# Kernel optimization log

Hardware: AMD Instinct MI355X
Metric: run time of the kernel (lower is better)

Reference implementation:

```python
import jax, jax.numpy as jnp
import numpy as np

TOP_K = 2  # num_experts_per_tok


def setup_inputs() -> dict:
    key = jax.random.key(0)
    ks = jax.random.split(key, 5)
    B, T, D, E, F = 2, 2048, 1024, 8, 2048
    scale_d = 1.0 / np.sqrt(D)
    scale_f = 1.0 / np.sqrt(F)
    return {
        "x": jax.random.normal(ks[0], (B, T, D), jnp.float32),
        "kernel_router_DE": jax.random.normal(ks[1], (D, E), jnp.float32) * scale_d,
        "kernel_gating_EDF": jax.random.normal(ks[2], (E, D, F), jnp.float32) * scale_d,
        "kernel_up_EDF": jax.random.normal(ks[3], (E, D, F), jnp.float32) * scale_d,
        "kernel_down_EFD": jax.random.normal(ks[4], (E, F, D), jnp.float32) * scale_f,
    }


def reference(x, kernel_router_DE, kernel_gating_EDF, kernel_up_EDF, kernel_down_EFD):
    E = kernel_router_DE.shape[-1]
    x = x.astype(jnp.float32)

    # --- Router: logits -> softmax -> top_k -> renormalize with softmax ---
    router_logits_BTE = jnp.einsum('BTD,DE->BTE', x, kernel_router_DE)
    probs_BTE = jax.nn.softmax(router_logits_BTE.astype(jnp.float32), axis=-1)
    weights_BTX, indices_BTX = jax.lax.top_k(probs_BTE, TOP_K)
    norm_weights_BTX = jax.nn.softmax(weights_BTX, axis=-1)

    # --- Scatter top-k weights back to dense per-expert weights ---
    one_hot_BTXE = jax.nn.one_hot(indices_BTX, num_classes=E, dtype=jnp.float32)
    full_weights_BTE = jnp.sum(one_hot_BTXE * norm_weights_BTX[..., None], axis=2)

    # --- Dense all-expert MLP (gating * up -> down), weighted combine ---
    gating_BTEF = jnp.einsum('BTD,EDF->BTEF', x, kernel_gating_EDF)
    fuse_BTEF = jax.nn.silu(gating_BTEF) * jnp.einsum('BTD,EDF->BTEF', x, kernel_up_EDF)
    down_BTED = jnp.einsum('BTEF,EFD->BTED', fuse_BTEF, kernel_down_EFD)
    out_BTD = jnp.einsum('BTED,BTE->BTD', down_BTED, full_weights_BTE)
    return out_BTD.astype(jnp.float32)
```

## Files before the change

### kernel.cpp

```cpp
#include <hip/hip_runtime.h>
#include <cstdint>

#define N_TOK 4096
#define DIM   1024
#define NEXP  8
#define FDIM  2048

typedef _Float16 f16_t;
typedef _Float16 f16x8 __attribute__((ext_vector_type(8)));
typedef float    f32x4 __attribute__((ext_vector_type(4)));

__device__ inline unsigned packh(float a, float b) {
    union { f16_t h[2]; unsigned u; } p;
    p.h[0] = (f16_t)a; p.h[1] = (f16_t)b;
    return p.u;
}

__device__ inline void gl2lds16(const void* g, void* l) {
    __builtin_amdgcn_global_load_lds(
        (const __attribute__((address_space(1))) unsigned*)g,
        (__attribute__((address_space(3))) unsigned*)l, 16, 0, 0);
}

__global__ __launch_bounds__(256) void prep_kernel(
    const float* __restrict__ x, const float* __restrict__ wr,
    float* __restrict__ topw, int* __restrict__ counts, int* __restrict__ bucket,
    f16_t* __restrict__ xf,
    const float* __restrict__ wg, const float* __restrict__ wu,
    f16_t* __restrict__ wgT, f16_t* __restrict__ wuT)
{
    __shared__ union { float r[NEXP][DIM]; unsigned sP[64][68]; } sm;
    __shared__ int sIdx[32];
    int tid = threadIdx.x;

    if (blockIdx.x >= 256) {
        int b2 = blockIdx.x - 256;
        int m = b2 >> 8;
        int tix = b2 & 255;
        const float* in; f16_t* out;
        if (m < 8) { in = wg + (size_t)m * DIM * FDIM;       out = wgT + (size_t)m * DIM * FDIM; }
        else       { in = wu + (size_t)(m - 8) * DIM * FDIM; out = wuT + (size_t)(m - 8) * DIM * FDIM; }
        int rb = (tix & 7) * 128;
        int cb = (tix >> 3) * 64;
        int dp = tid >> 2;
        int fc = (tid & 3) * 16;
        const float* r0 = in + (size_t)(rb + 2 * dp) * FDIM + cb + fc;
        const float* r1 = r0 + FDIM;
#pragma unroll
        for (int j = 0; j < 16; j += 4) {
            float4 a = *(const float4*)(r0 + j);
            float4 b = *(const float4*)(r1 + j);
            sm.sP[fc + j + 0][dp] = packh(a.x, b.x);
            sm.sP[fc + j + 1][dp] = packh(a.y, b.y);
            sm.sP[fc + j + 2][dp] = packh(a.z, b.z);
            sm.sP[fc + j + 3][dp] = packh(a.w, b.w);
        }
        __syncthreads();
        int c = tid >> 2;
        int rc = tid & 3;
        uint4* dst = (uint4*)(out + (size_t)(cb + c) * DIM + rb + rc * 32);
        const unsigned* src = &sm.sP[c][rc * 16];
#pragma unroll
        for (int j = 0; j < 4; j++)
            dst[j] = *(const uint4*)(src + j * 4);
        return;
    }

    int blk = blockIdx.x;
    {
        const float* xblk = x + (size_t)blk * 16 * DIM;
        f16_t* xfblk = xf + (size_t)blk * 16 * DIM;
#pragma unroll
        for (int i = tid; i < 16 * DIM / 8; i += 256) {
            float4 a = ((const float4*)xblk)[2 * i];
            float4 b = ((const float4*)xblk)[2 * i + 1];
            union { f16_t h[8]; uint4 u; } pk;
            pk.h[0] = (f16_t)a.x; pk.h[1] = (f16_t)a.y; pk.h[2] = (f16_t)a.z; pk.h[3] = (f16_t)a.w;
            pk.h[4] = (f16_t)b.x; pk.h[5] = (f16_t)b.y; pk.h[6] = (f16_t)b.z; pk.h[7] = (f16_t)b.w;
            ((uint4*)xfblk)[i] = pk.u;
        }
    }
    for (int i = tid; i < DIM * NEXP / 4; i += 256) {
        float4 v = ((const float4*)wr)[i];
        int base = i * 4;
        sm.r[(base + 0) & 7][(base + 0) >> 3] = v.x;
        sm.r[(base + 1) & 7][(base + 1) >> 3] = v.y;
        sm.r[(base + 2) & 7][(base + 2) >> 3] = v.z;
        sm.r[(base + 3) & 7][(base + 3) >> 3] = v.w;
    }
    __syncthreads();
    int wave = tid >> 6, lane = tid & 63;
    int t0 = blk * 16 + wave * 4;
    for (int tt = 0; tt < 4; ++tt) {
        int t = t0 + tt;
        float acc[NEXP];
#pragma unroll
        for (int e = 0; e < NEXP; e++) acc[e] = 0.f;
        const float* xr = x + (size_t)t * DIM;
#pragma unroll
        for (int k = 0; k < DIM / 64; k++) {
            int d = lane + k * 64;
            float xv = xr[d];
#pragma unroll
            for (int e = 0; e < NEXP; e++) acc[e] += xv * sm.r[e][d];
        }
#pragma unroll
        for (int e = 0; e < NEXP; e++) {
#pragma unroll
            for (int off = 32; off > 0; off >>= 1)
                acc[e] += __shfl_xor(acc[e], off, 64);
        }
        if (lane == 0) {
            float mx = acc[0];
#pragma unroll
            for (int e = 1; e < NEXP; e++) mx = fmaxf(mx, acc[e]);
            float p[NEXP]; float s = 0.f;
#pragma unroll
            for (int e = 0; e < NEXP; e++) { p[e] = expf(acc[e] - mx); s += p[e]; }
            float inv = 1.f / s;
#pragma unroll
            for (int e = 0; e < NEXP; e++) p[e] *= inv;
            int i1 = 0; float p1 = p[0];
#pragma unroll
            for (int e = 1; e < NEXP; e++) if (p[e] > p1) { p1 = p[e]; i1 = e; }
            int i2 = -1; float p2 = -1.f;
#pragma unroll
            for (int e = 0; e < NEXP; e++) if (e != i1 && p[e] > p2) { p2 = p[e]; i2 = e; }
            float e2 = expf(p2 - p1);
            float w1 = 1.f / (1.f + e2);
            topw[t * 2 + 0] = w1;
            topw[t * 2 + 1] = e2 * w1;
            int j = (wave * 4 + tt) * 2;
            sIdx[j + 0] = i1;
            sIdx[j + 1] = i2;
        }
    }
    __syncthreads();
    if (tid < NEXP) {
        int cnt = 0;
#pragma unroll
        for (int j = 0; j < 32; j++) cnt += (sIdx[j] == tid) ? 1 : 0;
        if (cnt > 0) {
            int pos = atomicAdd(&counts[tid * 32], cnt);
#pragma unroll
            for (int j = 0; j < 32; j++)
                if (sIdx[j] == tid)
                    bucket[tid * N_TOK + pos++] = (blk * 16 + (j >> 1)) * 2 + (j & 1);
        }
    }
}

__global__ __launch_bounds__(256) void gateup_kernel(
    const f16_t* __restrict__ xf,
    const f16_t* __restrict__ wgT, const f16_t* __restrict__ wuT,
    const int* __restrict__ counts, const int* __restrict__ bucket,
    f16_t* __restrict__ H)
{
    int flat = blockIdx.x;
    int e = flat & 7;
    int idx = flat >> 3;
    int m0 = (idx & 31) * 128;
    int n0 = (idx >> 5) * 64;
    int cnt = counts[e * 32];
    if (m0 >= cnt) return;

    __shared__ f16_t sA[128 * 32];
    __shared__ f16_t sBg[64 * 32];
    __shared__ f16_t sBu[64 * 32];
    __shared__ int sEnt[128];

    int tid = threadIdx.x;
    if (tid < 128) {
        int i = m0 + tid;
        sEnt[tid] = bucket[e * N_TOK + (i < cnt ? i : m0)];
    }
    __syncthreads();

    int wave = tid >> 6, lane = tid & 63;
    int q = ((lane & 3) - (lane >> 3)) & 3;
    int rA0 = wave * 32 + (lane >> 2);
    int rA1 = rA0 + 16;
    int rB  = wave * 16 + (lane >> 2);
    const f16_t* gA0 = xf + (size_t)(sEnt[rA0] >> 1) * DIM + q * 8;
    const f16_t* gA1 = xf + (size_t)(sEnt[rA1] >> 1) * DIM + q * 8;
    const f16_t* gBg = wgT + ((size_t)e * FDIM + n0 + rB) * DIM + q * 8;
    const f16_t* gBu = wuT + ((size_t)e * FDIM + n0 + rB) * DIM + q * 8;
    f16_t* lA0 = &sA[wave * 1024 + lane * 8];
    f16_t* lA1 = lA0 + 512;
    f16_t* lBg = &sBg[wave * 512 + lane * 8];
    f16_t* lBu = &sBu[wave * 512 + lane * 8];

    f32x4 accG[4][2], accU[4][2];
    f32x4 zero = {0.f, 0.f, 0.f, 0.f};
#pragma unroll
    for (int i = 0; i < 4; i++)
#pragma unroll
        for (int j = 0; j < 2; j++) { accG[i][j] = zero; accU[i][j] = zero; }

    int wm = (wave & 1) * 64, wn = (wave >> 1) * 32;
    int fm = lane & 15, quad = lane >> 4;
    int p8 = ((quad + (fm >> 1)) & 3) * 8;

    for (int k0 = 0; k0 < DIM; k0 += 32) {
        gl2lds16(gA0 + k0, lA0);
        gl2lds16(gA1 + k0, lA1);
        gl2lds16(gBg + k0, lBg);
        gl2lds16(gBu + k0, lBu);
        __syncthreads();
        f16x8 af[4], bg[2], bu[2];
#pragma unroll
        for (int mi = 0; mi < 4; mi++)
            af[mi] = *(const f16x8*)&sA[(wm + mi * 16 + fm) * 32 + p8];
#pragma unroll
        for (int ni = 0; ni < 2; ni++) {
            bg[ni] = *(const f16x8*)&sBg[(wn + ni * 16 + fm) * 32 + p8];
            bu[ni] = *(const f16x8*)&sBu[(wn + ni * 16 + fm) * 32 + p8];
        }
#pragma unroll
        for (int mi = 0; mi < 4; mi++)
#pragma unroll
            for (int ni = 0; ni < 2; ni++) {
                accG[mi][ni] = __builtin_amdgcn_mfma_f32_16x16x32_f16(af[mi], bg[ni], accG[mi][ni], 0, 0, 0);
                accU[mi][ni] = __builtin_amdgcn_mfma_f32_16x16x32_f16(af[mi], bu[ni], accU[mi][ni], 0, 0, 0);
            }
        __syncthreads();
    }
    int crow = quad * 4, ccol = fm;
#pragma unroll
    for (int mi = 0; mi < 4; mi++) {
#pragma unroll
        for (int i = 0; i < 4; i++) {
            int m = wm + mi * 16 + crow + i;
            if (m0 + m < cnt) {
                int ent = sEnt[m];
                f16_t* hr = H + (size_t)ent * FDIM + n0 + wn;
#pragma unroll
                for (int ni = 0; ni < 2; ni++) {
                    float g = accG[mi][ni][i], u = accU[mi][ni][i];
                    float h = (g / (1.f + __expf(-g))) * u;
                    hr[ni * 16 + ccol] = (f16_t)h;
                }
            }
        }
    }
}

__global__ __launch_bounds__(256) void down_kernel(
    const f16_t* __restrict__ H, const float* __restrict__ wd,
    const int* __restrict__ counts, const int* __restrict__ bucket,
    const float* __restrict__ topw, float* __restrict__ out)
{
    int flat = blockIdx.x;
    int e = flat & 7;
    int idx = flat >> 3;
    int m0 = (idx & 31) * 128;
    int n0 = (idx >> 5) * 128;
    int cnt = counts[e * 32];
    if (m0 >= cnt) return;

    __shared__ f16_t sA[128 * 32];
    __shared__ f16_t sB[128 * 32];
    __shared__ int sEnt[128];

    int tid = threadIdx.x;
    if (tid < 128) {
        int i = m0 + tid;
        sEnt[tid] = bucket[e * N_TOK + (i < cnt ? i : m0)];
    }
    __syncthreads();

    int wave = tid >> 6, lane = tid & 63;
    int q = ((lane & 3) - (lane >> 3)) & 3;
    int r0 = wave * 32 + (lane >> 2);
    int r1 = r0 + 16;
    const f16_t* gA0 = H + (size_t)sEnt[r0] * FDIM + q * 8;
    const f16_t* gA1 = H + (size_t)sEnt[r1] * FDIM + q * 8;
    f16_t* lA0 = &sA[wave * 1024 + lane * 8];
    f16_t* lA1 = lA0 + 512;

    int fp = tid & 7;
    int dq = tid >> 3;
    int fp2 = fp * 2;
    const float* wde = wd + (size_t)e * FDIM * DIM + n0 + dq * 4;
    int o2 = (fp & 3) * 2;
    int g0 = (fp >> 2);
    int g1 = 2 + (fp >> 2);
    int cA = ((g0 ^ (dq & 3)) * 8) + o2;
    int cB = ((g1 ^ (dq & 3)) * 8) + o2;
    int rowb = dq * 4;

    float4 pb0, pb1, pb2, pb3;
#define LOADB(K0) {                                                             \
        const float* rr = wde + (size_t)((K0) + fp2) * DIM;                     \
        pb0 = *(const float4*)rr;                                               \
        pb1 = *(const float4*)(rr + DIM);                                       \
        pb2 = *(const float4*)(rr + 16 * DIM);                                  \
        pb3 = *(const float4*)(rr + 17 * DIM); }

    f32x4 acc[4][4];
    f32x4 zero = {0.f, 0.f, 0.f, 0.f};
#pragma unroll
    for (int i = 0; i < 4; i++)
#pragma unroll
        for (int j = 0; j < 4; j++) acc[i][j] = zero;

    int wm = (wave & 1) * 64, wn = (wave >> 1) * 64;
    int fm = lane & 15, quad = lane >> 4;
    int p8 = ((quad + (fm >> 1)) & 3) * 8;

    LOADB(0);
    for (int k0 = 0; k0 < FDIM; k0 += 32) {
        gl2lds16(gA0 + k0, lA0);
        gl2lds16(gA1 + k0, lA1);
        *(unsigned*)&sB[(rowb + 0) * 32 + cA] = packh(pb0.x, pb1.x);
        *(unsigned*)&sB[(rowb + 1) * 32 + cA] = packh(pb0.y, pb1.y);
        *(unsigned*)&sB[(rowb + 2) * 32 + cA] = packh(pb0.z, pb1.z);
        *(unsigned*)&sB[(rowb + 3) * 32 + cA] = packh(pb0.w, pb1.w);
        *(unsigned*)&sB[(rowb + 0) * 32 + cB] = packh(pb2.x, pb3.x);
        *(unsigned*)&sB[(rowb + 1) * 32 + cB] = packh(pb2.y, pb3.y);
        *(unsigned*)&sB[(rowb + 2) * 32 + cB] = packh(pb2.z, pb3.z);
        *(unsigned*)&sB[(rowb + 3) * 32 + cB] = packh(pb2.w, pb3.w);
        __syncthreads();
        if (k0 + 32 < FDIM) LOADB(k0 + 32);
        f16x8 af[4], bf[4];
#pragma unroll
        for (int mi = 0; mi < 4; mi++)
            af[mi] = *(const f16x8*)&sA[(wm + mi * 16 + fm) * 32 + p8];
#pragma unroll
        for (int ni = 0; ni < 4; ni++) {
            int row = wn + ni * 16 + fm;
            bf[ni] = *(const f16x8*)&sB[row * 32 + (quad ^ ((row >> 2) & 3)) * 8];
        }
#pragma unroll
        for (int mi = 0; mi < 4; mi++)
#pragma unroll
            for (int ni = 0; ni < 4; ni++)
                acc[mi][ni] = __builtin_amdgcn_mfma_f32_16x16x32_f16(af[mi], bf[ni], acc[mi][ni], 0, 0, 0);
        __syncthreads();
    }
#undef LOADB

    int crow = quad * 4, ccol = fm;
#pragma unroll
    for (int mi = 0; mi < 4; mi++) {
#pragma unroll
        for (int i = 0; i < 4; i++) {
            int m = wm + mi * 16 + crow + i;
            if (m0 + m < cnt) {
                int ent = sEnt[m];
                float w = topw[ent];
                float* orow = out + (size_t)(ent >> 1) * DIM + n0 + wn;
#pragma unroll
                for (int ni = 0; ni < 4; ni++)
                    atomicAdd(&orow[ni * 16 + ccol], w * acc[mi][ni][i]);
            }
        }
    }
}

extern "C" void kernel_launch(void* const* d_in, const int* in_sizes, int n_in,
                              void* d_out, int out_size, void* d_ws, size_t ws_size,
                              hipStream_t stream) {
    const float* x  = (const float*)d_in[0];
    const float* wr = (const float*)d_in[1];
    const float* wg = (const float*)d_in[2];
    const float* wu = (const float*)d_in[3];
    const float* wd = (const float*)d_in[4];
    float* out = (float*)d_out;
    char* ws = (char*)d_ws;
    const size_t MB = 1ull << 20;

    int*   counts = (int*)ws;
    int*   bucket = (int*)(ws + 1024);
    float* topw   = (float*)(ws + 160 * 1024);
    f16_t* xf     = (f16_t*)(ws + 1 * MB);
    f16_t* wgT    = (f16_t*)(ws + 9 * MB);
    f16_t* wuT    = (f16_t*)(ws + 41 * MB);
    f16_t* H      = (f16_t*)(ws + 73 * MB);

    hipMemsetAsync(counts, 0, 1024, stream);
    hipMemsetAsync(out, 0, out_size, stream);
    prep_kernel<<<4352, 256, 0, stream>>>(x, wr, topw, counts, bucket, xf, wg, wu, wgT, wuT);
    gateup_kernel<<<8192, 256, 0, stream>>>(xf, wgT, wuT, counts, bucket, H);
    down_kernel<<<2048, 256, 0, stream>>>(H, wd, counts, bucket, topw, out);
}
```

Baseline: 444.7 us.

## Pre-convert down-projection weights to transposed fp16 before the down GEMM

The down-projection weights are now converted once per call into a transposed fp16 copy. This happens either inside the prep kernel, when the workspace is large enough, or in a separate conversion kernel that reuses the xf region. The down kernel then streams the B operand with direct global-to-LDS loads, in place of register-staged fp32 loads that were repacked in every k-iteration. This cuts the per-tile fp32 traffic and repack work, since the conversion is not repeated across the many M-tiles. In exchange it adds a full weight conversion pass and extra workspace traffic.

```diff
diff --git a/kernel.cpp b/kernel.cpp
--- a/kernel.cpp
+++ b/kernel.cpp
@@ -27,7 +27,8 @@
     float* __restrict__ topw, int* __restrict__ counts, int* __restrict__ bucket,
     f16_t* __restrict__ xf,
     const float* __restrict__ wg, const float* __restrict__ wu,
-    f16_t* __restrict__ wgT, f16_t* __restrict__ wuT)
+    const float* __restrict__ wd,
+    f16_t* __restrict__ wgT, f16_t* __restrict__ wuT, f16_t* __restrict__ wdT)
 {
     __shared__ union { float r[NEXP][DIM]; unsigned sP[64][68]; } sm;
     __shared__ int sIdx[32];
@@ -38,14 +39,22 @@
         int m = b2 >> 8;
         int tix = b2 & 255;
         const float* in; f16_t* out;
-        if (m < 8) { in = wg + (size_t)m * DIM * FDIM;       out = wgT + (size_t)m * DIM * FDIM; }
-        else       { in = wu + (size_t)(m - 8) * DIM * FDIM; out = wuT + (size_t)(m - 8) * DIM * FDIM; }
-        int rb = (tix & 7) * 128;
-        int cb = (tix >> 3) * 64;
+        int R, C, tiles_r;
+        if (m < 16) {
+            R = DIM; C = FDIM; tiles_r = DIM / 128;
+            if (m < 8) { in = wg + (size_t)m * DIM * FDIM;       out = wgT + (size_t)m * DIM * FDIM; }
+            else       { in = wu + (size_t)(m - 8) * DIM * FDIM; out = wuT + (size_t)(m - 8) * DIM * FDIM; }
+        } else {
+            R = FDIM; C = DIM; tiles_r = FDIM / 128;
+            in = wd + (size_t)(m - 16) * FDIM * DIM;
+            out = wdT + (size_t)(m - 16) * FDIM * DIM;
+        }
+        int rb = (tix % tiles_r) * 128;
+        int cb = (tix / tiles_r) * 64;
         int dp = tid >> 2;
         int fc = (tid & 3) * 16;
-        const float* r0 = in + (size_t)(rb + 2 * dp) * FDIM + cb + fc;
-        const float* r1 = r0 + FDIM;
+        const float* r0 = in + (size_t)(rb + 2 * dp) * C + cb + fc;
+        const float* r1 = r0 + C;
 #pragma unroll
         for (int j = 0; j < 16; j += 4) {
             float4 a = *(const float4*)(r0 + j);
@@ -58,7 +67,7 @@
         __syncthreads();
         int c = tid >> 2;
         int rc = tid & 3;
-        uint4* dst = (uint4*)(out + (size_t)(cb + c) * DIM + rb + rc * 32);
+        uint4* dst = (uint4*)(out + (size_t)(cb + c) * R + rb + rc * 32);
         const unsigned* src = &sm.sP[c][rc * 16];
 #pragma unroll
         for (int j = 0; j < 4; j++)
@@ -148,6 +157,41 @@
                     bucket[tid * N_TOK + pos++] = (blk * 16 + (j >> 1)) * 2 + (j & 1);
         }
     }
+}
+
+__global__ __launch_bounds__(256) void wdcvt_kernel(
+    const float* __restrict__ wd, f16_t* __restrict__ wdT)
+{
+    __shared__ unsigned sP[64][68];
+    int m = blockIdx.y;
+    const float* in = wd + (size_t)m * FDIM * DIM;
+    f16_t* out = wdT + (size_t)m * FDIM * DIM;
+    int tix = blockIdx.x;
+    int tiles_r = FDIM / 128;
+    int rb = (tix % tiles_r) * 128;
+    int cb = (tix / tiles_r) * 64;
+    int t = threadIdx.x;
+    int dp = t >> 2;
+    int fc = (t & 3) * 16;
+    const float* r0 = in + (size_t)(rb + 2 * dp) * DIM + cb + fc;
+    const float* r1 = r0 + DIM;
+#pragma unroll
+    for (int j = 0; j < 16; j += 4) {
+        float4 a = *(const float4*)(r0 + j);
+        float4 b = *(const float4*)(r1 + j);
+        sP[fc + j + 0][dp] = packh(a.x, b.x);
+        sP[fc + j + 1][dp] = packh(a.y, b.y);
+        sP[fc + j + 2][dp] = packh(a.z, b.z);
+        sP[fc + j + 3][dp] = packh(a.w, b.w);
+    }
+    __syncthreads();
+    int c = t >> 2;
+    int rc = t & 3;
+    uint4* dst = (uint4*)(out + (size_t)(cb + c) * FDIM + rb + rc * 32);
+    const unsigned* src = &sP[c][rc * 16];
+#pragma unroll
+    for (int j = 0; j < 4; j++)
+        dst[j] = *(const uint4*)(src + j * 4);
 }
 
 __global__ __launch_bounds__(256) void gateup_kernel(
@@ -246,7 +290,7 @@
 }
 
 __global__ __launch_bounds__(256) void down_kernel(
-    const f16_t* __restrict__ H, const float* __restrict__ wd,
+    const f16_t* __restrict__ H, const f16_t* __restrict__ wdT,
     const int* __restrict__ counts, const int* __restrict__ bucket,
     const float* __restrict__ topw, float* __restrict__ out)
 {
@@ -275,27 +319,12 @@
     int r1 = r0 + 16;
     const f16_t* gA0 = H + (size_t)sEnt[r0] * FDIM + q * 8;
     const f16_t* gA1 = H + (size_t)sEnt[r1] * FDIM + q * 8;
+    const f16_t* gB0 = wdT + ((size_t)e * DIM + n0 + r0) * FDIM + q * 8;
+    const f16_t* gB1 = wdT + ((size_t)e * DIM + n0 + r1) * FDIM + q * 8;
     f16_t* lA0 = &sA[wave * 1024 + lane * 8];
     f16_t* lA1 = lA0 + 512;
-
-    int fp = tid & 7;
-    int dq = tid >> 3;
-    int fp2 = fp * 2;
-    const float* wde = wd + (size_t)e * FDIM * DIM + n0 + dq * 4;
-    int o2 = (fp & 3) * 2;
-    int g0 = (fp >> 2);
-    int g1 = 2 + (fp >> 2);
-    int cA = ((g0 ^ (dq & 3)) * 8) + o2;
-    int cB = ((g1 ^ (dq & 3)) * 8) + o2;
-    int rowb = dq * 4;
-
-    float4 pb0, pb1, pb2, pb3;
-#define LOADB(K0) {                                                             \
-        const float* rr = wde + (size_t)((K0) + fp2) * DIM;                     \
-        pb0 = *(const float4*)rr;                                               \
-        pb1 = *(const float4*)(rr + DIM);                                       \
-        pb2 = *(const float4*)(rr + 16 * DIM);                                  \
-        pb3 = *(const float4*)(rr + 17 * DIM); }
+    f16_t* lB0 = &sB[wave * 1024 + lane * 8];
+    f16_t* lB1 = lB0 + 512;
 
     f32x4 acc[4][4];
     f32x4 zero = {0.f, 0.f, 0.f, 0.f};
@@ -308,29 +337,19 @@
     int fm = lane & 15, quad = lane >> 4;
     int p8 = ((quad + (fm >> 1)) & 3) * 8;
 
-    LOADB(0);
     for (int k0 = 0; k0 < FDIM; k0 += 32) {
         gl2lds16(gA0 + k0, lA0);
         gl2lds16(gA1 + k0, lA1);
-        *(unsigned*)&sB[(rowb + 0) * 32 + cA] = packh(pb0.x, pb1.x);
-        *(unsigned*)&sB[(rowb + 1) * 32 + cA] = packh(pb0.y, pb1.y);
-        *(unsigned*)&sB[(rowb + 2) * 32 + cA] = packh(pb0.z, pb1.z);
-        *(unsigned*)&sB[(rowb + 3) * 32 + cA] = packh(pb0.w, pb1.w);
-        *(unsigned*)&sB[(rowb + 0) * 32 + cB] = packh(pb2.x, pb3.x);
-        *(unsigned*)&sB[(rowb + 1) * 32 + cB] = packh(pb2.y, pb3.y);
-        *(unsigned*)&sB[(rowb + 2) * 32 + cB] = packh(pb2.z, pb3.z);
-        *(unsigned*)&sB[(rowb + 3) * 32 + cB] = packh(pb2.w, pb3.w);
+        gl2lds16(gB0 + k0, lB0);
+        gl2lds16(gB1 + k0, lB1);
         __syncthreads();
-        if (k0 + 32 < FDIM) LOADB(k0 + 32);
         f16x8 af[4], bf[4];
 #pragma unroll
         for (int mi = 0; mi < 4; mi++)
             af[mi] = *(const f16x8*)&sA[(wm + mi * 16 + fm) * 32 + p8];
 #pragma unroll
-        for (int ni = 0; ni < 4; ni++) {
-            int row = wn + ni * 16 + fm;
-            bf[ni] = *(const f16x8*)&sB[row * 32 + (quad ^ ((row >> 2) & 3)) * 8];
-        }
+        for (int ni = 0; ni < 4; ni++)
+            bf[ni] = *(const f16x8*)&sB[(wn + ni * 16 + fm) * 32 + p8];
 #pragma unroll
         for (int mi = 0; mi < 4; mi++)
 #pragma unroll
@@ -338,8 +357,6 @@
                 acc[mi][ni] = __builtin_amdgcn_mfma_f32_16x16x32_f16(af[mi], bf[ni], acc[mi][ni], 0, 0, 0);
         __syncthreads();
     }
-#undef LOADB
-
     int crow = quad * 4, ccol = fm;
 #pragma unroll
     for (int mi = 0; mi < 4; mi++) {
@@ -378,9 +395,16 @@
     f16_t* wuT    = (f16_t*)(ws + 41 * MB);
     f16_t* H      = (f16_t*)(ws + 73 * MB);
 
+    bool big = ws_size >= 137 * MB;
+    f16_t* wdT = big ? (f16_t*)(ws + 105 * MB) : (f16_t*)(ws + 1 * MB);
+
     hipMemsetAsync(counts, 0, 1024, stream);
     hipMemsetAsync(out, 0, out_size, stream);
-    prep_kernel<<<4352, 256, 0, stream>>>(x, wr, topw, counts, bucket, xf, wg, wu, wgT, wuT);
+    int prep_blocks = 256 + 16 * 256 + (big ? 8 * 256 : 0);
+    prep_kernel<<<prep_blocks, 256, 0, stream>>>(x, wr, topw, counts, bucket, xf,
+                                                 wg, wu, wd, wgT, wuT, wdT);
     gateup_kernel<<<8192, 256, 0, stream>>>(xf, wgT, wuT, counts, bucket, H);
-    down_kernel<<<2048, 256, 0, stream>>>(H, wd, counts, bucket, topw, out);
-}
+    if (!big)
+        wdcvt_kernel<<<dim3(256, 8), 256, 0, stream>>>(wd, wdT);
+    down_kernel<<<2048, 256, 0, stream>>>(H, wdT, counts, bucket, topw, out);
+}
```

Result: faster. 409.5 us (-7.9%).
